# Kernel optimization log

Hardware: AMD Instinct MI355X
Metric: run time of the kernel (lower is better)

The kernel has to match this reference:

```python
import jax, jax.numpy as jnp
import numpy as np

B, H, W, D = 8, 16, 512, 512
N_HEADS = 8
D_HEAD = D // N_HEADS
LN_EPS = 1e-5


def _make_pe(H_, W_, D_):
    # Mirrors the torch 2D sinusoidal PE construction (sliced to [:H,:W]).
    half = D_ // 2
    den = np.power(10000.0, np.arange(0, half, 2, dtype=np.float32) / D_)  # [D/4]
    pos_h = np.arange(H_, dtype=np.float32)[:, None]  # [H,1]
    pos_w = np.arange(W_, dtype=np.float32)[:, None]  # [W,1]
    pe = np.zeros((H_, W_, D_), dtype=np.float32)
    pe[:, :, 0:half:2] = np.sin(pos_w / den)[None, :, :]
    pe[:, :, 1:half:2] = np.cos(pos_w / den)[None, :, :]
    pe[:, :, half::2] = np.sin(pos_h / den)[:, None, :]
    pe[:, :, half + 1::2] = np.cos(pos_h / den)[:, None, :]
    return jnp.asarray(pe)


def setup_inputs() -> dict:
    key = jax.random.key(0)
    ks = jax.random.split(key, 8)
    swin_2d = jax.random.normal(ks[0], (B, H, W, D), dtype=jnp.float32)
    pe = _make_pe(H, W, D)
    pitch_queries = 0.02 * jax.random.normal(ks[1], (N_HEADS, D_HEAD), dtype=jnp.float32)
    k_w = 0.02 * jax.random.normal(ks[2], (D, H), dtype=jnp.float32)  # depthwise conv weight [D,1,H] squeezed
    k_b = jnp.zeros((D,), dtype=jnp.float32)
    kp_w = 0.02 * jax.random.normal(ks[3], (D, D), dtype=jnp.float32)
    kp_b = 0.02 * jax.random.normal(ks[4], (D,), dtype=jnp.float32)
    vp_w = 0.02 * jax.random.normal(ks[5], (D, D), dtype=jnp.float32)
    vp_b = 0.02 * jax.random.normal(ks[6], (D,), dtype=jnp.float32)
    ln_g = jnp.ones((D,), dtype=jnp.float32)
    ln_b = jnp.zeros((D,), dtype=jnp.float32)
    return {"swin_2d": swin_2d, "pe": pe, "pitch_queries": pitch_queries,
            "k_w": k_w, "k_b": k_b, "kp_w": kp_w, "kp_b": kp_b,
            "vp_w": vp_w, "vp_b": vp_b, "ln_g": ln_g, "ln_b": ln_b}


def reference(swin_2d, pe, pitch_queries, k_w, k_b, kp_w, kp_b, vp_w, vp_b, ln_g, ln_b):
    B_, H_, W_, D_ = swin_2d.shape
    nh, dh = pitch_queries.shape
    x = swin_2d + pe[None]                               # [B,H,W,D] positional add
    x = jnp.transpose(x, (0, 2, 1, 3)).reshape(B_ * W_, H_, D_)  # [BW,H,D]
    # depthwise Conv1d over H (kernel_size=H, groups=D) == per-channel weighted sum
    memory_k = (jnp.einsum('nhd,dh->nd', x, k_w) + k_b).reshape(B_, W_, D_)
    # k/v projections (nn.Linear: x @ W.T + b)
    k = (x @ kp_w.T + kp_b).reshape(B_ * W_, H_, nh, dh)  # [BW,H,heads,dh]
    v = (x @ vp_w.T + vp_b).reshape(B_ * W_, H_, nh, dh)
    # cross-attention: 1 learned query per head attends over H freq bins
    scale = 1.0 / jnp.sqrt(jnp.asarray(dh, dtype=x.dtype))
    scores = jnp.einsum('nfed,ed->nef', k, pitch_queries) * scale  # [BW,heads,H]
    attn = jax.nn.softmax(scores, axis=-1)
    pitch_out = jnp.einsum('nef,nfed->ned', attn, v).reshape(B_, W_, D_)
    # LayerNorm over D
    mu = jnp.mean(pitch_out, axis=-1, keepdims=True)
    var = jnp.mean(jnp.square(pitch_out - mu), axis=-1, keepdims=True)
    memory_v = (pitch_out - mu) * jax.lax.rsqrt(var + LN_EPS) * ln_g + ln_b
    return (memory_k, memory_v)
```

## Files before the change

kernel.cpp:

```cpp
#include <hip/hip_runtime.h>

typedef unsigned int  uint32;
typedef unsigned short u16;

__device__ __forceinline__ uint32 pk2(float a, float b){
  union {float f; uint32 i;} x, y; x.f = a; y.f = b;
  uint32 lo = ((x.i + 0x7fffu + ((x.i >> 16) & 1u)) >> 16);
  uint32 hi = ((y.i + 0x7fffu + ((y.i >> 16) & 1u)) & 0xffff0000u);
  return lo | hi;
}
__device__ __forceinline__ void unp8(uint4 v, float* f){
  union {uint32 i; float x;} a;
  a.i = v.x << 16;         f[0] = a.x;
  a.i = v.x & 0xffff0000u; f[1] = a.x;
  a.i = v.y << 16;         f[2] = a.x;
  a.i = v.y & 0xffff0000u; f[3] = a.x;
  a.i = v.z << 16;         f[4] = a.x;
  a.i = v.z & 0xffff0000u; f[5] = a.x;
  a.i = v.w << 16;         f[6] = a.x;
  a.i = v.w & 0xffff0000u; f[7] = a.x;
}

__global__ __launch_bounds__(256) void k0_qk(const float* __restrict__ pq,
    const float* __restrict__ kpw, const float* __restrict__ kpb,
    float* __restrict__ qkw, float* __restrict__ qkb){
  int e = blockIdx.x >> 1;
  int d = ((blockIdx.x & 1) << 8) + threadIdx.x;
  float acc = 0.f;
  #pragma unroll 8
  for (int j = 0; j < 64; j++){
    int row = e * 64 + j;
    acc += pq[row] * kpw[(size_t)row * 512 + d];
  }
  qkw[e * 512 + d] = acc * 0.125f;
  if (blockIdx.x == 0 && threadIdx.x < 8){
    int ee = threadIdx.x;
    float a = 0.f;
    for (int j = 0; j < 64; j++) a += pq[ee*64 + j] * kpb[ee*64 + j];
    qkb[ee] = a * 0.125f;
  }
}

#define XLD 516
__global__ __launch_bounds__(256) void k1_main(const float* __restrict__ swin,
    const float* __restrict__ pe, const float* __restrict__ kw, const float* __restrict__ kb,
    const float* __restrict__ qkw, const float* __restrict__ qkb,
    float* __restrict__ outk, u16* __restrict__ y){
  __shared__ float xs[16 * XLD];
  __shared__ float sc[128];
  __shared__ float at[128];
  const int tid = threadIdx.x;
  const int n = blockIdx.x;
  const int b = n >> 9, w = n & 511;

  {
    const float4* s4 = (const float4*)swin;
    const float4* p4 = (const float4*)pe;
    const size_t sbase = (size_t)b * 16 * 65536 + (size_t)w * 128;
    const size_t pbase = (size_t)w * 128;
    #pragma unroll
    for (int i = 0; i < 8; i++){
      int f = i * 256 + tid;
      int h = f >> 7, c4 = f & 127;
      float4 av = s4[sbase + (size_t)h * 65536 + c4];
      float4 pv = p4[pbase + (size_t)h * 65536 + c4];
      float* dst = &xs[h * XLD + c4 * 4];
      dst[0] = av.x + pv.x; dst[1] = av.y + pv.y;
      dst[2] = av.z + pv.z; dst[3] = av.w + pv.w;
    }
  }
  __syncthreads();

  #pragma unroll
  for (int r = 0; r < 2; r++){
    int d = (r << 8) + tid;
    const float4* kr = (const float4*)kw + d * 4;
    float kf[16];
    *(float4*)&kf[0]  = kr[0]; *(float4*)&kf[4]  = kr[1];
    *(float4*)&kf[8]  = kr[2]; *(float4*)&kf[12] = kr[3];
    float acc = kb[d];
    #pragma unroll
    for (int h = 0; h < 16; h++) acc += xs[h * XLD + d] * kf[h];
    outk[(size_t)n * 512 + d] = acc;
  }

  {
    int p = tid >> 1, half = tid & 1;
    int e = p >> 4, h = p & 15;
    const float*  xr = &xs[h * XLD + (half << 8)];
    const float4* qr = (const float4*)&qkw[e * 512 + (half << 8)];
    float acc = 0.f;
    #pragma unroll 8
    for (int i = 0; i < 64; i++){
      float4 xv = *(const float4*)&xr[i * 4];
      float4 qv = qr[i];
      acc += xv.x*qv.x + xv.y*qv.y + xv.z*qv.z + xv.w*qv.w;
    }
    acc += __shfl_xor(acc, 1);
    if (!half) sc[p] = acc + qkb[e];
  }
  __syncthreads();

  if (tid < 8){
    float m = -1e30f;
    #pragma unroll
    for (int h = 0; h < 16; h++) m = fmaxf(m, sc[tid*16 + h]);
    float ex[16]; float s = 0.f;
    #pragma unroll
    for (int h = 0; h < 16; h++){ ex[h] = __expf(sc[tid*16 + h] - m); s += ex[h]; }
    float inv = 1.f / s;
    #pragma unroll
    for (int h = 0; h < 16; h++) at[tid*16 + h] = ex[h] * inv;
  }
  __syncthreads();

  {
    int wv = tid >> 6, lane = tid & 63;
    int e0 = wv << 1;
    float ar0[16], ar1[16];
    #pragma unroll
    for (int h = 0; h < 16; h++){ ar0[h] = at[e0*16 + h]; ar1[h] = at[e0*16 + 16 + h]; }
    int da = lane << 2, db = 256 + (lane << 2);
    float a00[4] = {0,0,0,0}, a01[4] = {0,0,0,0}, a10[4] = {0,0,0,0}, a11[4] = {0,0,0,0};
    #pragma unroll
    for (int h = 0; h < 16; h++){
      float4 x0 = *(const float4*)&xs[h * XLD + da];
      float4 x1 = *(const float4*)&xs[h * XLD + db];
      float c0 = ar0[h], c1 = ar1[h];
      a00[0] += c0*x0.x; a00[1] += c0*x0.y; a00[2] += c0*x0.z; a00[3] += c0*x0.w;
      a01[0] += c0*x1.x; a01[1] += c0*x1.y; a01[2] += c0*x1.z; a01[3] += c0*x1.w;
      a10[0] += c1*x0.x; a10[1] += c1*x0.y; a10[2] += c1*x0.z; a10[3] += c1*x0.w;
      a11[0] += c1*x1.x; a11[1] += c1*x1.y; a11[2] += c1*x1.z; a11[3] += c1*x1.w;
    }
    size_t ybase = (size_t)n * 4096;
    uint2 s0;
    s0.x = pk2(a00[0], a00[1]); s0.y = pk2(a00[2], a00[3]);
    *(uint2*)&y[ybase + (size_t)e0 * 512 + da] = s0;
    s0.x = pk2(a01[0], a01[1]); s0.y = pk2(a01[2], a01[3]);
    *(uint2*)&y[ybase + (size_t)e0 * 512 + db] = s0;
    s0.x = pk2(a10[0], a10[1]); s0.y = pk2(a10[2], a10[3]);
    *(uint2*)&y[ybase + (size_t)(e0+1) * 512 + da] = s0;
    s0.x = pk2(a11[0], a11[1]); s0.y = pk2(a11[2], a11[3]);
    *(uint2*)&y[ybase + (size_t)(e0+1) * 512 + db] = s0;
  }
}

__global__ __launch_bounds__(512) void k2_v(const u16* __restrict__ y,
    const float* __restrict__ vpw, const float* __restrict__ vpb,
    const float* __restrict__ lng, const float* __restrict__ lnb,
    float* __restrict__ outv){
  __shared__ u16 ys[8 * 4096];
  const int tid = threadIdx.x;
  const size_t n0 = (size_t)blockIdx.x * 8;

  {
    const uint4* src = (const uint4*)(y + n0 * 4096);
    uint4* dst = (uint4*)ys;
    #pragma unroll
    for (int i = 0; i < 8; i++) dst[i * 512 + tid] = src[i * 512 + tid];
  }
  __syncthreads();

  const int dout = tid;
  const int e = dout >> 6;
  float acc[8];
  float bias = vpb[dout];
  #pragma unroll
  for (int nn = 0; nn < 8; nn++) acc[nn] = bias;

  const float4* vr = (const float4*)vpw + dout * 128;
  const uint4*  yb = (const uint4*)ys + (e << 6);
  for (int d8 = 0; d8 < 64; d8++){
    float wf[8];
    *(float4*)&wf[0] = vr[d8 * 2];
    *(float4*)&wf[4] = vr[d8 * 2 + 1];
    #pragma unroll
    for (int nn = 0; nn < 8; nn++){
      float yf[8];
      unp8(yb[nn * 512 + d8], yf);
      acc[nn] += yf[0]*wf[0] + yf[1]*wf[1] + yf[2]*wf[2] + yf[3]*wf[3]
               + yf[4]*wf[4] + yf[5]*wf[5] + yf[6]*wf[6] + yf[7]*wf[7];
    }
  }
  __syncthreads();

  float* ps = (float*)ys;
  #pragma unroll
  for (int nn = 0; nn < 8; nn++) ps[nn * 512 + dout] = acc[nn];
  __syncthreads();

  {
    int wv = tid >> 6, lane = tid & 63;
    float vals[8]; float s1 = 0.f, s2 = 0.f;
    #pragma unroll
    for (int j = 0; j < 8; j++){
      float v = ps[wv * 512 + lane + (j << 6)];
      vals[j] = v; s1 += v; s2 += v * v;
    }
    #pragma unroll
    for (int o = 1; o < 64; o <<= 1){ s1 += __shfl_xor(s1, o); s2 += __shfl_xor(s2, o); }
    float mu  = s1 * (1.f / 512.f);
    float var = s2 * (1.f / 512.f) - mu * mu;
    float inv = 1.f / sqrtf(var + 1e-5f);
    float* dst = outv + 2097152 + ((size_t)n0 + wv) * 512;
    #pragma unroll
    for (int j = 0; j < 8; j++){
      int d = lane + (j << 6);
      dst[d] = (vals[j] - mu) * inv * lng[d] + lnb[d];
    }
  }
}

extern "C" void kernel_launch(void* const* d_in, const int* in_sizes, int n_in,
                              void* d_out, int out_size, void* d_ws, size_t ws_size,
                              hipStream_t stream) {
  const float* swin = (const float*)d_in[0];
  const float* pe   = (const float*)d_in[1];
  const float* pq   = (const float*)d_in[2];
  const float* kw   = (const float*)d_in[3];
  const float* kb   = (const float*)d_in[4];
  const float* kpw  = (const float*)d_in[5];
  const float* kpb  = (const float*)d_in[6];
  const float* vpw  = (const float*)d_in[7];
  const float* vpb  = (const float*)d_in[8];
  const float* lng  = (const float*)d_in[9];
  const float* lnb  = (const float*)d_in[10];
  float* out = (float*)d_out;

  float* qkw = (float*)d_ws;
  float* qkb = qkw + 4096;
  u16*   y   = (u16*)((char*)d_ws + 32768);

  k0_qk  <<<16,   256, 0, stream>>>(pq, kpw, kpb, qkw, qkb);
  k1_main<<<4096, 256, 0, stream>>>(swin, pe, kw, kb, qkw, qkb, out, y);
  k2_v   <<<512,  512, 0, stream>>>(y, vpw, vpb, lng, lnb, out);
}
```

Measured before the change: 348.1 us.

## Use bf16 MFMA GEMM for V projection, store x tile as bf16 in LDS

Replaces the scalar FMA V-projection kernel with a bf16 MFMA tiled GEMM per head, on weights pre-converted to bf16 by a new kernel, followed by a separate LayerNorm kernel. The main kernel now keeps the positional-added input tile in LDS as bf16 rather than fp32, halving shared memory per block to raise occupancy. The GEMM is meant to remove the ALU-bound projection cost. In exchange it adds a float intermediate round trip through global memory, two extra launches, and bf16 rounding of the input, which affects memory_k accuracy.

```diff
diff --git a/kernel.cpp b/kernel.cpp
--- a/kernel.cpp
+++ b/kernel.cpp
@@ -2,7 +2,12 @@
 
 typedef unsigned int  uint32;
 typedef unsigned short u16;
-
+typedef __attribute__((ext_vector_type(8))) short short8x;
+typedef __attribute__((ext_vector_type(4))) float f32x4;
+
+__device__ __forceinline__ float bf2f(u16 u){
+  union {uint32 i; float f;} v; v.i = ((uint32)u) << 16; return v.f;
+}
 __device__ __forceinline__ uint32 pk2(float a, float b){
   union {float f; uint32 i;} x, y; x.f = a; y.f = b;
   uint32 lo = ((x.i + 0x7fffu + ((x.i >> 16) & 1u)) >> 16);
@@ -41,12 +46,23 @@
   }
 }
 
-#define XLD 516
+__global__ __launch_bounds__(256) void k0b_cvt(const float* __restrict__ vpw,
+    u16* __restrict__ wb){
+  int g = blockIdx.x * 256 + threadIdx.x;
+  const float4* s = (const float4*)vpw + (size_t)g * 2;
+  float4 a = s[0], b = s[1];
+  uint4 o;
+  o.x = pk2(a.x, a.y); o.y = pk2(a.z, a.w);
+  o.z = pk2(b.x, b.y); o.w = pk2(b.z, b.w);
+  ((uint4*)wb)[g] = o;
+}
+
+#define LDX 520
 __global__ __launch_bounds__(256) void k1_main(const float* __restrict__ swin,
     const float* __restrict__ pe, const float* __restrict__ kw, const float* __restrict__ kb,
     const float* __restrict__ qkw, const float* __restrict__ qkb,
     float* __restrict__ outk, u16* __restrict__ y){
-  __shared__ float xs[16 * XLD];
+  __shared__ u16 xs[16 * LDX];
   __shared__ float sc[128];
   __shared__ float at[128];
   const int tid = threadIdx.x;
@@ -59,14 +75,18 @@
     const size_t sbase = (size_t)b * 16 * 65536 + (size_t)w * 128;
     const size_t pbase = (size_t)w * 128;
     #pragma unroll
-    for (int i = 0; i < 8; i++){
-      int f = i * 256 + tid;
-      int h = f >> 7, c4 = f & 127;
-      float4 av = s4[sbase + (size_t)h * 65536 + c4];
-      float4 pv = p4[pbase + (size_t)h * 65536 + c4];
-      float* dst = &xs[h * XLD + c4 * 4];
-      dst[0] = av.x + pv.x; dst[1] = av.y + pv.y;
-      dst[2] = av.z + pv.z; dst[3] = av.w + pv.w;
+    for (int i = 0; i < 4; i++){
+      int g = i * 256 + tid;
+      int h = g >> 6, c8 = g & 63;
+      size_t o = (size_t)h * 65536 + c8 * 2;
+      float4 a0 = s4[sbase + o],     p0 = p4[pbase + o];
+      float4 a1 = s4[sbase + o + 1], p1 = p4[pbase + o + 1];
+      uint4 pk;
+      pk.x = pk2(a0.x + p0.x, a0.y + p0.y);
+      pk.y = pk2(a0.z + p0.z, a0.w + p0.w);
+      pk.z = pk2(a1.x + p1.x, a1.y + p1.y);
+      pk.w = pk2(a1.z + p1.z, a1.w + p1.w);
+      *(uint4*)&xs[h * LDX + c8 * 8] = pk;
     }
   }
   __syncthreads();
@@ -80,21 +100,23 @@
     *(float4*)&kf[8]  = kr[2]; *(float4*)&kf[12] = kr[3];
     float acc = kb[d];
     #pragma unroll
-    for (int h = 0; h < 16; h++) acc += xs[h * XLD + d] * kf[h];
+    for (int h = 0; h < 16; h++) acc += bf2f(xs[h * LDX + d]) * kf[h];
     outk[(size_t)n * 512 + d] = acc;
   }
 
   {
     int p = tid >> 1, half = tid & 1;
     int e = p >> 4, h = p & 15;
-    const float*  xr = &xs[h * XLD + (half << 8)];
+    const uint4*  xr = (const uint4*)&xs[h * LDX + (half << 8)];
     const float4* qr = (const float4*)&qkw[e * 512 + (half << 8)];
     float acc = 0.f;
-    #pragma unroll 8
-    for (int i = 0; i < 64; i++){
-      float4 xv = *(const float4*)&xr[i * 4];
-      float4 qv = qr[i];
-      acc += xv.x*qv.x + xv.y*qv.y + xv.z*qv.z + xv.w*qv.w;
+    #pragma unroll 4
+    for (int i = 0; i < 32; i++){
+      float xf[8];
+      unp8(xr[i], xf);
+      float4 q0 = qr[i * 2], q1 = qr[i * 2 + 1];
+      acc += xf[0]*q0.x + xf[1]*q0.y + xf[2]*q0.z + xf[3]*q0.w
+           + xf[4]*q1.x + xf[5]*q1.y + xf[6]*q1.z + xf[7]*q1.w;
     }
     acc += __shfl_xor(acc, 1);
     if (!half) sc[p] = acc + qkb[e];
@@ -120,95 +142,119 @@
     float ar0[16], ar1[16];
     #pragma unroll
     for (int h = 0; h < 16; h++){ ar0[h] = at[e0*16 + h]; ar1[h] = at[e0*16 + 16 + h]; }
-    int da = lane << 2, db = 256 + (lane << 2);
-    float a00[4] = {0,0,0,0}, a01[4] = {0,0,0,0}, a10[4] = {0,0,0,0}, a11[4] = {0,0,0,0};
+    float a0[8] = {0,0,0,0,0,0,0,0}, a1[8] = {0,0,0,0,0,0,0,0};
+    const int da = lane << 3;
     #pragma unroll
     for (int h = 0; h < 16; h++){
-      float4 x0 = *(const float4*)&xs[h * XLD + da];
-      float4 x1 = *(const float4*)&xs[h * XLD + db];
+      uint4 xv = *(const uint4*)&xs[h * LDX + da];
+      float xf[8];
+      unp8(xv, xf);
       float c0 = ar0[h], c1 = ar1[h];
-      a00[0] += c0*x0.x; a00[1] += c0*x0.y; a00[2] += c0*x0.z; a00[3] += c0*x0.w;
-      a01[0] += c0*x1.x; a01[1] += c0*x1.y; a01[2] += c0*x1.z; a01[3] += c0*x1.w;
-      a10[0] += c1*x0.x; a10[1] += c1*x0.y; a10[2] += c1*x0.z; a10[3] += c1*x0.w;
-      a11[0] += c1*x1.x; a11[1] += c1*x1.y; a11[2] += c1*x1.z; a11[3] += c1*x1.w;
-    }
-    size_t ybase = (size_t)n * 4096;
-    uint2 s0;
-    s0.x = pk2(a00[0], a00[1]); s0.y = pk2(a00[2], a00[3]);
-    *(uint2*)&y[ybase + (size_t)e0 * 512 + da] = s0;
-    s0.x = pk2(a01[0], a01[1]); s0.y = pk2(a01[2], a01[3]);
-    *(uint2*)&y[ybase + (size_t)e0 * 512 + db] = s0;
-    s0.x = pk2(a10[0], a10[1]); s0.y = pk2(a10[2], a10[3]);
-    *(uint2*)&y[ybase + (size_t)(e0+1) * 512 + da] = s0;
-    s0.x = pk2(a11[0], a11[1]); s0.y = pk2(a11[2], a11[3]);
-    *(uint2*)&y[ybase + (size_t)(e0+1) * 512 + db] = s0;
-  }
-}
-
-__global__ __launch_bounds__(512) void k2_v(const u16* __restrict__ y,
-    const float* __restrict__ vpw, const float* __restrict__ vpb,
+      #pragma unroll
+      for (int j = 0; j < 8; j++){ a0[j] += c0 * xf[j]; a1[j] += c1 * xf[j]; }
+    }
+    size_t ybase = (size_t)n * 4096 + da;
+    uint4 o;
+    o.x = pk2(a0[0],a0[1]); o.y = pk2(a0[2],a0[3]);
+    o.z = pk2(a0[4],a0[5]); o.w = pk2(a0[6],a0[7]);
+    *(uint4*)&y[ybase + (size_t)e0 * 512] = o;
+    o.x = pk2(a1[0],a1[1]); o.y = pk2(a1[2],a1[3]);
+    o.z = pk2(a1[4],a1[5]); o.w = pk2(a1[6],a1[7]);
+    *(uint4*)&y[ybase + (size_t)(e0+1) * 512] = o;
+  }
+}
+
+#define LDK 136
+__global__ __launch_bounds__(256) void k2_gemm(const u16* __restrict__ y,
+    const u16* __restrict__ wb, const float* __restrict__ vpb,
+    float* __restrict__ pout){
+  __shared__ u16 As[64 * LDK];
+  __shared__ u16 Bs[64 * LDK];
+  const int tid = threadIdx.x;
+  const int e = blockIdx.x >> 6, nt = blockIdx.x & 63;
+  const int n0 = nt * 64;
+  const int wv = tid >> 6, lane = tid & 63;
+  const int mrow = (wv >> 1) * 32, ncol = (wv & 1) * 32;
+  const int lr = lane & 15, lk = (lane >> 4) * 8;
+  f32x4 acc[2][2] = {{{0.f,0.f,0.f,0.f},{0.f,0.f,0.f,0.f}},
+                     {{0.f,0.f,0.f,0.f},{0.f,0.f,0.f,0.f}}};
+  const int sr = tid >> 2, seg = tid & 3;
+
+  for (int kc = 0; kc < 4; kc++){
+    const u16* ga = y  + (size_t)(n0 + sr) * 4096 + e * 512 + kc * 128 + seg * 32;
+    const u16* gb = wb + (size_t)(e * 64 + sr) * 512 + kc * 128 + seg * 32;
+    u16* la = &As[sr * LDK + seg * 32];
+    u16* lb = &Bs[sr * LDK + seg * 32];
+    #pragma unroll
+    for (int u = 0; u < 4; u++){
+      *(uint4*)(la + u * 8) = *(const uint4*)(ga + u * 8);
+      *(uint4*)(lb + u * 8) = *(const uint4*)(gb + u * 8);
+    }
+    __syncthreads();
+    #pragma unroll
+    for (int kk = 0; kk < 4; kk++){
+      int kb = kk * 32 + lk;
+      short8x af[2], bf[2];
+      #pragma unroll
+      for (int m = 0; m < 2; m++)
+        af[m] = *(const short8x*)&As[(mrow + m * 16 + lr) * LDK + kb];
+      #pragma unroll
+      for (int nq = 0; nq < 2; nq++)
+        bf[nq] = *(const short8x*)&Bs[(ncol + nq * 16 + lr) * LDK + kb];
+      #pragma unroll
+      for (int m = 0; m < 2; m++)
+        #pragma unroll
+        for (int nq = 0; nq < 2; nq++)
+          acc[m][nq] = __builtin_amdgcn_mfma_f32_16x16x32_bf16(
+              af[m], bf[nq], acc[m][nq], 0, 0, 0);
+    }
+    __syncthreads();
+  }
+  #pragma unroll
+  for (int m = 0; m < 2; m++){
+    int gn = n0 + mrow + m * 16 + (lane >> 4) * 4;
+    #pragma unroll
+    for (int nq = 0; nq < 2; nq++){
+      int gd = e * 64 + ncol + nq * 16 + lr;
+      float bias = vpb[gd];
+      #pragma unroll
+      for (int j = 0; j < 4; j++)
+        pout[(size_t)(gn + j) * 512 + gd] = acc[m][nq][j] + bias;
+    }
+  }
+}
+
+__global__ __launch_bounds__(256) void k3_ln(const float* __restrict__ pout,
     const float* __restrict__ lng, const float* __restrict__ lnb,
     float* __restrict__ outv){
-  __shared__ u16 ys[8 * 4096];
-  const int tid = threadIdx.x;
-  const size_t n0 = (size_t)blockIdx.x * 8;
-
-  {
-    const uint4* src = (const uint4*)(y + n0 * 4096);
-    uint4* dst = (uint4*)ys;
-    #pragma unroll
-    for (int i = 0; i < 8; i++) dst[i * 512 + tid] = src[i * 512 + tid];
-  }
-  __syncthreads();
-
-  const int dout = tid;
-  const int e = dout >> 6;
-  float acc[8];
-  float bias = vpb[dout];
+  const int row  = blockIdx.x * 4 + (threadIdx.x >> 6);
+  const int lane = threadIdx.x & 63;
+  const float4* src = (const float4*)(pout + (size_t)row * 512);
+  float4 v0 = src[lane * 2], v1 = src[lane * 2 + 1];
+  float s1 = v0.x + v0.y + v0.z + v0.w + v1.x + v1.y + v1.z + v1.w;
+  float s2 = v0.x*v0.x + v0.y*v0.y + v0.z*v0.z + v0.w*v0.w
+           + v1.x*v1.x + v1.y*v1.y + v1.z*v1.z + v1.w*v1.w;
   #pragma unroll
-  for (int nn = 0; nn < 8; nn++) acc[nn] = bias;
-
-  const float4* vr = (const float4*)vpw + dout * 128;
-  const uint4*  yb = (const uint4*)ys + (e << 6);
-  for (int d8 = 0; d8 < 64; d8++){
-    float wf[8];
-    *(float4*)&wf[0] = vr[d8 * 2];
-    *(float4*)&wf[4] = vr[d8 * 2 + 1];
-    #pragma unroll
-    for (int nn = 0; nn < 8; nn++){
-      float yf[8];
-      unp8(yb[nn * 512 + d8], yf);
-      acc[nn] += yf[0]*wf[0] + yf[1]*wf[1] + yf[2]*wf[2] + yf[3]*wf[3]
-               + yf[4]*wf[4] + yf[5]*wf[5] + yf[6]*wf[6] + yf[7]*wf[7];
-    }
-  }
-  __syncthreads();
-
-  float* ps = (float*)ys;
-  #pragma unroll
-  for (int nn = 0; nn < 8; nn++) ps[nn * 512 + dout] = acc[nn];
-  __syncthreads();
-
-  {
-    int wv = tid >> 6, lane = tid & 63;
-    float vals[8]; float s1 = 0.f, s2 = 0.f;
-    #pragma unroll
-    for (int j = 0; j < 8; j++){
-      float v = ps[wv * 512 + lane + (j << 6)];
-      vals[j] = v; s1 += v; s2 += v * v;
-    }
-    #pragma unroll
-    for (int o = 1; o < 64; o <<= 1){ s1 += __shfl_xor(s1, o); s2 += __shfl_xor(s2, o); }
-    float mu  = s1 * (1.f / 512.f);
-    float var = s2 * (1.f / 512.f) - mu * mu;
-    float inv = 1.f / sqrtf(var + 1e-5f);
-    float* dst = outv + 2097152 + ((size_t)n0 + wv) * 512;
-    #pragma unroll
-    for (int j = 0; j < 8; j++){
-      int d = lane + (j << 6);
-      dst[d] = (vals[j] - mu) * inv * lng[d] + lnb[d];
-    }
-  }
+  for (int o = 1; o < 64; o <<= 1){ s1 += __shfl_xor(s1, o); s2 += __shfl_xor(s2, o); }
+  float mu  = s1 * (1.f / 512.f);
+  float var = s2 * (1.f / 512.f) - mu * mu;
+  float inv = 1.f / sqrtf(var + 1e-5f);
+  const int d0 = lane * 8;
+  const float4* g4 = (const float4*)(lng + d0);
+  const float4* b4 = (const float4*)(lnb + d0);
+  float4 g0 = g4[0], g1 = g4[1], bb0 = b4[0], bb1 = b4[1];
+  float* dst = outv + 2097152 + (size_t)row * 512 + d0;
+  float4 o0, o1;
+  o0.x = (v0.x - mu) * inv * g0.x + bb0.x;
+  o0.y = (v0.y - mu) * inv * g0.y + bb0.y;
+  o0.z = (v0.z - mu) * inv * g0.z + bb0.z;
+  o0.w = (v0.w - mu) * inv * g0.w + bb0.w;
+  o1.x = (v1.x - mu) * inv * g1.x + bb1.x;
+  o1.y = (v1.y - mu) * inv * g1.y + bb1.y;
+  o1.z = (v1.z - mu) * inv * g1.z + bb1.z;
+  o1.w = (v1.w - mu) * inv * g1.w + bb1.w;
+  *(float4*)dst       = o0;
+  *(float4*)(dst + 4) = o1;
 }
 
 extern "C" void kernel_launch(void* const* d_in, const int* in_sizes, int n_in,
@@ -227,11 +273,15 @@
   const float* lnb  = (const float*)d_in[10];
   float* out = (float*)d_out;
 
-  float* qkw = (float*)d_ws;
-  float* qkb = qkw + 4096;
-  u16*   y   = (u16*)((char*)d_ws + 32768);
+  float* qkw  = (float*)d_ws;
+  float* qkb  = qkw + 4096;
+  u16*   y    = (u16*)((char*)d_ws + 32768);
+  u16*   wbuf = (u16*)((char*)d_ws + 32768 + 33554432);
+  float* pout = (float*)((char*)d_ws + 32768 + 33554432 + 524288);
 
   k0_qk  <<<16,   256, 0, stream>>>(pq, kpw, kpb, qkw, qkb);
+  k0b_cvt<<<128,  256, 0, stream>>>(vpw, wbuf);
   k1_main<<<4096, 256, 0, stream>>>(swin, pe, kw, kb, qkw, qkb, out, y);
-  k2_v   <<<512,  512, 0, stream>>>(y, vpw, vpb, lng, lnb, out);
-}
+  k2_gemm<<<512,  256, 0, stream>>>(y, wbuf, vpb, pout);
+  k3_ln  <<<1024, 256, 0, stream>>>(pout, lng, lnb, out);
+}
```

New measurement: 292.0 us. -16.1%, faster.
